# Kernel optimization log

Measured on AMD Instinct MI355X. Metric: run time of the kernel, lower is better.

The kernel has to match this reference:

```python
import jax, jax.numpy as jnp
import numpy as np


def _dsepconv(inp, vertical, horizontal, offset_x, offset_y, mask):
    # inp: [B,C,H,W]; vertical/horizontal: [B,F,H,W]; offset_x/offset_y/mask: [B,F*F,H,W]
    B, C, H, W = inp.shape
    F_ = min(vertical.shape[1], horizontal.shape[1])
    T = F_ * F_
    out_h = min(vertical.shape[2], horizontal.shape[2])
    out_w = min(vertical.shape[3], horizontal.shape[3])

    fy = jnp.repeat(jnp.arange(F_), F_).astype(inp.dtype)   # [T] tap row index
    fx = jnp.tile(jnp.arange(F_), F_).astype(inp.dtype)     # [T] tap col index
    h_idx = jnp.arange(out_h, dtype=inp.dtype)
    w_idx = jnp.arange(out_w, dtype=inp.dtype)
    c_off = (F_ - 1) / 2.0

    # NOTE: original code uses offset_y for the x coordinate and offset_x for y (faithful swap)
    x_norm = 2.0 * (offset_y + w_idx[None, None, None, :] + fx[None, :, None, None] - c_off + 1.0) / W - 1.0
    y_norm = 2.0 * (offset_x + h_idx[None, None, :, None] + fy[None, :, None, None] - c_off + 1.0) / H - 1.0
    x_norm = jnp.clip(x_norm, -1.0, 1.0)
    y_norm = jnp.clip(y_norm, -1.0, 1.0)

    # grid_sample align_corners=False mapping to pixel coords
    ix = ((x_norm + 1.0) * W - 1.0) / 2.0   # [B,T,H,W]
    iy = ((y_norm + 1.0) * H - 1.0) / 2.0

    x0 = jnp.floor(ix)
    y0 = jnp.floor(iy)
    wx1 = ix - x0  # fractional weights
    wy1 = iy - y0
    wx0 = 1.0 - wx1
    wy0 = 1.0 - wy1

    # border padding: clamp integer neighbor indices
    x0i = jnp.clip(x0.astype(jnp.int32), 0, W - 1)
    x1i = jnp.clip(x0.astype(jnp.int32) + 1, 0, W - 1)
    y0i = jnp.clip(y0.astype(jnp.int32), 0, H - 1)
    y1i = jnp.clip(y0.astype(jnp.int32) + 1, 0, H - 1)

    def gather(img, yi, xi):  # img [C,H,W], yi/xi [T,h,w] -> [C,T,h,w]
        return img[:, yi, xi]
    g = jax.vmap(gather)  # over batch -> [B,C,T,h,w]

    # combined per-tap coefficient: vertical[fy] * horizontal[fx] * mask[tap]
    coef = (vertical[:, jnp.repeat(jnp.arange(F_), F_), :out_h, :out_w]
            * horizontal[:, jnp.tile(jnp.arange(F_), F_), :out_h, :out_w]
            * mask[:, :, :out_h, :out_w])  # [B,T,h,w]

    out = (jnp.einsum('bthw,bcthw->bchw', coef * wy0 * wx0, g(inp, y0i, x0i))
           + jnp.einsum('bthw,bcthw->bchw', coef * wy0 * wx1, g(inp, y0i, x1i))
           + jnp.einsum('bthw,bcthw->bchw', coef * wy1 * wx0, g(inp, y1i, x0i))
           + jnp.einsum('bthw,bcthw->bchw', coef * wy1 * wx1, g(inp, y1i, x1i)))
    return out


def setup_inputs() -> dict:
    key = jax.random.key(0)
    k = jax.random.split(key, 6)
    B, C, H, W, F_ = 2, 3, 512, 512, 5
    T = F_ * F_
    return {
        'tensorInput': jax.random.normal(k[0], (B, C, H, W), dtype=jnp.float32),
        'tensorVertical': jax.random.uniform(k[1], (B, F_, H, W), dtype=jnp.float32),
        'tensorHorizontal': jax.random.uniform(k[2], (B, F_, H, W), dtype=jnp.float32),
        'tensorOffsetX': jax.random.normal(k[3], (B, T, H, W), dtype=jnp.float32),
        'tensorOffsetY': jax.random.normal(k[4], (B, T, H, W), dtype=jnp.float32),
        'tensorMask': jax.random.uniform(k[5], (B, T, H, W), dtype=jnp.float32),
    }


def reference(tensorInput, tensorVertical, tensorHorizontal, tensorOffsetX, tensorOffsetY, tensorMask):
    return _dsepconv(tensorInput, tensorVertical, tensorHorizontal, tensorOffsetX, tensorOffsetY, tensorMask)
```

## Files before the change

### kernel.cpp

```cpp
#include <hip/hip_runtime.h>

#define B_ 2
#define C_ 3
#define H_ 512
#define W_ 512
#define F_ 5
#define T_ 25
#define HW_ (H_ * W_)
#define PW_ 520
#define PH_ 513

#define NT(p) __builtin_nontemporal_load(p)

typedef _Float16 h4 __attribute__((ext_vector_type(4), aligned(8)));
typedef _Float16 h8 __attribute__((ext_vector_type(8), aligned(8)));

__global__ __launch_bounds__(256) void repack_kernel(
    const float* __restrict__ inp, h4* __restrict__ pk)
{
    const int x   = (blockIdx.x << 8) + threadIdx.x;
    const int row = blockIdx.y;
    const int b   = blockIdx.z;
    const int sr  = row < H_ ? row : H_ - 1;
    const float* p = inp + b * (C_ * HW_) + (sr << 9) + x;
    h4 v;
    v.x = (_Float16)p[0];
    v.y = (_Float16)p[HW_];
    v.z = (_Float16)p[2 * HW_];
    v.w = (_Float16)0.f;
    h4* dst = pk + b * (PH_ * PW_) + row * PW_;
    dst[x] = v;
    if (x == W_ - 1) dst[W_] = v;
}

__global__ __launch_bounds__(256) void dsepconv_kernel(
    const h4* __restrict__ pk,
    const float* __restrict__ vert,
    const float* __restrict__ horz,
    const float* __restrict__ offx,
    const float* __restrict__ offy,
    const float* __restrict__ mask,
    float* __restrict__ out)
{
    const int idx = blockIdx.x * blockDim.x + threadIdx.x;
    const int w = idx & (W_ - 1);
    const int h = (idx >> 9) & (H_ - 1);
    const int b = idx >> 18;

    const int hw = (h << 9) | w;

    const float* vb   = vert + b * (F_ * HW_) + hw;
    const float* hb   = horz + b * (F_ * HW_) + hw;
    const float* ob_x = offx + b * (T_ * HW_) + hw;
    const float* ob_y = offy + b * (T_ * HW_) + hw;
    const float* mb   = mask + b * (T_ * HW_) + hw;
    const h4* pb      = pk + b * (PH_ * PW_);

    float v[F_], hz[F_];
#pragma unroll
    for (int f = 0; f < F_; ++f) v[f]  = NT(vb + f * HW_);
#pragma unroll
    for (int f = 0; f < F_; ++f) hz[f] = NT(hb + f * HW_);

    float acc0 = 0.f, acc1 = 0.f, acc2 = 0.f;

    const float wf = (float)w;
    const float hf = (float)h;

    float cy[F_], cx[F_], cm[F_];
#pragma unroll
    for (int fx = 0; fx < F_; ++fx) {
        cy[fx] = NT(ob_y + fx * HW_);
        cx[fx] = NT(ob_x + fx * HW_);
        cm[fx] = NT(mb   + fx * HW_);
    }

#pragma unroll
    for (int fy = 0; fy < F_; ++fy) {
        float ny[F_], nx[F_], nm[F_];
        if (fy < F_ - 1) {
#pragma unroll
            for (int fx = 0; fx < F_; ++fx) {
                const int t = (fy + 1) * F_ + fx;
                ny[fx] = NT(ob_y + t * HW_);
                nx[fx] = NT(ob_x + t * HW_);
                nm[fx] = NT(mb   + t * HW_);
            }
        }

        const float vfy = v[fy];
        const float fyf = (float)fy;

#pragma unroll
        for (int fx = 0; fx < F_; ++fx) {
            const float oy = cy[fx];
            const float ox = cx[fx];
            const float m  = cm[fx];

            float ixf = oy + (wf + (float)fx - 1.5f);
            float iyf = ox + (hf + fyf       - 1.5f);
            ixf = fminf(fmaxf(ixf, -0.5f), (float)W_ - 0.5f);
            iyf = fminf(fmaxf(iyf, -0.5f), (float)H_ - 0.5f);

            float x0f = floorf(ixf), y0f = floorf(iyf);
            float wx1 = (x0f < 0.f) ? 0.f : (ixf - x0f);
            float wy1 = (y0f < 0.f) ? 0.f : (iyf - y0f);
            float wx0 = 1.0f - wx1;

            const int xb = (int)fmaxf(x0f, 0.f);
            const int yb = (int)fmaxf(y0f, 0.f);

            const h8 gt = *(const h8*)(pb + yb * PW_ + xb);
            const h8 gb = *(const h8*)(pb + (yb + 1) * PW_ + xb);

            const float coef = vfy * hz[fx] * m;
            const float cw0 = coef * (1.0f - wy1);
            const float cw1 = coef * wy1;

            const float t0 = wx0 * (float)gt[0] + wx1 * (float)gt[4];
            const float t1 = wx0 * (float)gt[1] + wx1 * (float)gt[5];
            const float t2 = wx0 * (float)gt[2] + wx1 * (float)gt[6];
            const float b0 = wx0 * (float)gb[0] + wx1 * (float)gb[4];
            const float b1 = wx0 * (float)gb[1] + wx1 * (float)gb[5];
            const float b2 = wx0 * (float)gb[2] + wx1 * (float)gb[6];

            acc0 += cw0 * t0 + cw1 * b0;
            acc1 += cw0 * t1 + cw1 * b1;
            acc2 += cw0 * t2 + cw1 * b2;
        }

        if (fy < F_ - 1) {
#pragma unroll
            for (int fx = 0; fx < F_; ++fx) {
                cy[fx] = ny[fx];
                cx[fx] = nx[fx];
                cm[fx] = nm[fx];
            }
        }
    }

    float* ob = out + b * (C_ * HW_) + hw;
    __builtin_nontemporal_store(acc0, ob);
    __builtin_nontemporal_store(acc1, ob + HW_);
    __builtin_nontemporal_store(acc2, ob + 2 * HW_);
}

extern "C" void kernel_launch(void* const* d_in, const int* in_sizes, int n_in,
                              void* d_out, int out_size, void* d_ws, size_t ws_size,
                              hipStream_t stream) {
    const float* inp  = (const float*)d_in[0];
    const float* vert = (const float*)d_in[1];
    const float* horz = (const float*)d_in[2];
    const float* offx = (const float*)d_in[3];
    const float* offy = (const float*)d_in[4];
    const float* mask = (const float*)d_in[5];
    float* out = (float*)d_out;
    h4* pk = (h4*)d_ws;

    dim3 blockR(256), gridR(W_ / 256, PH_, B_);
    hipLaunchKernelGGL(repack_kernel, gridR, blockR, 0, stream, inp, pk);

    const int total = B_ * H_ * W_;
    dim3 block(256), grid(total / 256);
    hipLaunchKernelGGL(dsepconv_kernel, grid, block, 0, stream,
                       pk, vert, horz, offx, offy, mask, out);
}
```

Before: 207.3 us.

## Stage input halo tile in LDS for bilinear gathers with global fallback

The kernel now runs on a 2D grid of 64x4 pixel blocks. Each block first copies a 25x88 packed fp16 halo region of the input into shared memory, then serves the bilinear corner gathers from LDS, falling back to global memory when a sampled offset lands outside the halo. The goal is to replace scattered global/L2 gathers with LDS reads. In exchange it adds a tile-load phase, a barrier, about 17.6KB of LDS per block and divergent fallback branches. It also raises the launch bounds minimum occupancy hint.

```diff
diff --git a/kernel.cpp b/kernel.cpp
--- a/kernel.cpp
+++ b/kernel.cpp
@@ -10,10 +10,17 @@
 #define PW_ 520
 #define PH_ 513
 
+#define TBW 64
+#define TBH 4
+#define RY  10
+#define RX  10
+#define TRH (TBH + 2 * RY + 1)
+#define TCW 88
+#define TILE_N (TRH * TCW)
+
 #define NT(p) __builtin_nontemporal_load(p)
 
 typedef _Float16 h4 __attribute__((ext_vector_type(4), aligned(8)));
-typedef _Float16 h8 __attribute__((ext_vector_type(8), aligned(8)));
 
 __global__ __launch_bounds__(256) void repack_kernel(
     const float* __restrict__ inp, h4* __restrict__ pk)
@@ -33,7 +40,7 @@
     if (x == W_ - 1) dst[W_] = v;
 }
 
-__global__ __launch_bounds__(256) void dsepconv_kernel(
+__global__ __launch_bounds__(256, 4) void dsepconv_kernel(
     const h4* __restrict__ pk,
     const float* __restrict__ vert,
     const float* __restrict__ horz,
@@ -42,10 +49,15 @@
     const float* __restrict__ mask,
     float* __restrict__ out)
 {
-    const int idx = blockIdx.x * blockDim.x + threadIdx.x;
-    const int w = idx & (W_ - 1);
-    const int h = (idx >> 9) & (H_ - 1);
-    const int b = idx >> 18;
+    __shared__ h4 tile[TILE_N];
+
+    const int tid  = threadIdx.x;
+    const int lane = tid & 63;
+    const int h0   = blockIdx.y * TBH;
+    const int w0b  = blockIdx.x * TBW;
+    const int b    = blockIdx.z;
+    const int h    = h0 + (tid >> 6);
+    const int w    = w0b + lane;
 
     const int hw = (h << 9) | w;
 
@@ -62,11 +74,6 @@
 #pragma unroll
     for (int f = 0; f < F_; ++f) hz[f] = NT(hb + f * HW_);
 
-    float acc0 = 0.f, acc1 = 0.f, acc2 = 0.f;
-
-    const float wf = (float)w;
-    const float hf = (float)h;
-
     float cy[F_], cx[F_], cm[F_];
 #pragma unroll
     for (int fx = 0; fx < F_; ++fx) {
@@ -74,6 +81,22 @@
         cx[fx] = NT(ob_x + fx * HW_);
         cm[fx] = NT(mb   + fx * HW_);
     }
+
+    for (int j = tid; j < TILE_N; j += 256) {
+        const int r  = j / TCW;
+        const int c  = j - r * TCW;
+        const int gr = min(max(h0 - RY + r, 0), H_);
+        const int gc = min(max(w0b - RX + c, 0), W_);
+        tile[j] = pb[gr * PW_ + gc];
+    }
+    __syncthreads();
+
+    float acc0 = 0.f, acc1 = 0.f, acc2 = 0.f;
+
+    const float wf = (float)w;
+    const float hf = (float)h;
+    const int hm = h0 - RY;
+    const int wm = w0b - RX;
 
 #pragma unroll
     for (int fy = 0; fy < F_; ++fy) {
@@ -110,23 +133,34 @@
             const int xb = (int)fmaxf(x0f, 0.f);
             const int yb = (int)fmaxf(y0f, 0.f);
 
-            const h8 gt = *(const h8*)(pb + yb * PW_ + xb);
-            const h8 gb = *(const h8*)(pb + (yb + 1) * PW_ + xb);
+            const int ty = yb - hm;
+            const int tc = xb - wm;
+
+            h4 t00, t01, t10, t11;
+            if (__builtin_expect((unsigned)ty < (TRH - 1) && (unsigned)tc < (TCW - 1), 1)) {
+                const h4* p = &tile[ty * TCW + tc];
+                t00 = p[0];
+                t01 = p[1];
+                t10 = p[TCW];
+                t11 = p[TCW + 1];
+            } else {
+                const h4* gp = pb + yb * PW_ + xb;
+                t00 = gp[0];
+                t01 = gp[1];
+                t10 = gp[PW_];
+                t11 = gp[PW_ + 1];
+            }
 
             const float coef = vfy * hz[fx] * m;
             const float cw0 = coef * (1.0f - wy1);
             const float cw1 = coef * wy1;
 
-            const float t0 = wx0 * (float)gt[0] + wx1 * (float)gt[4];
-            const float t1 = wx0 * (float)gt[1] + wx1 * (float)gt[5];
-            const float t2 = wx0 * (float)gt[2] + wx1 * (float)gt[6];
-            const float b0 = wx0 * (float)gb[0] + wx1 * (float)gb[4];
-            const float b1 = wx0 * (float)gb[1] + wx1 * (float)gb[5];
-            const float b2 = wx0 * (float)gb[2] + wx1 * (float)gb[6];
-
-            acc0 += cw0 * t0 + cw1 * b0;
-            acc1 += cw0 * t1 + cw1 * b1;
-            acc2 += cw0 * t2 + cw1 * b2;
+            acc0 += cw0 * (wx0 * (float)t00.x + wx1 * (float)t01.x)
+                  + cw1 * (wx0 * (float)t10.x + wx1 * (float)t11.x);
+            acc1 += cw0 * (wx0 * (float)t00.y + wx1 * (float)t01.y)
+                  + cw1 * (wx0 * (float)t10.y + wx1 * (float)t11.y);
+            acc2 += cw0 * (wx0 * (float)t00.z + wx1 * (float)t01.z)
+                  + cw1 * (wx0 * (float)t10.z + wx1 * (float)t11.z);
         }
 
         if (fy < F_ - 1) {
@@ -160,8 +194,8 @@
     dim3 blockR(256), gridR(W_ / 256, PH_, B_);
     hipLaunchKernelGGL(repack_kernel, gridR, blockR, 0, stream, inp, pk);
 
-    const int total = B_ * H_ * W_;
-    dim3 block(256), grid(total / 256);
+    dim3 block(256);
+    dim3 grid(W_ / TBW, H_ / TBH, B_);
     hipLaunchKernelGGL(dsepconv_kernel, grid, block, 0, stream,
                        pk, vert, horz, offx, offy, mask, out);
 }
```

After: 440.6 us. 2.13x slower.

## Do bilinear interpolation in packed fp16 and drop manual load prefetching

Applied to the files above, without the earlier changes.

The bilinear blend of the four gathered pixels now runs as packed half-precision vector math: horizontal lerp, then vertical lerp, then one fp32 multiply by the tap coefficient per channel. The manual double-buffering of next-row offset and mask loads is removed, so each row's loads are issued just before use. Launch bounds now request 4 waves per SIMD to limit register use. This aims to cut ALU work and register pressure, in exchange for fp16 rounding in the interpolation weights and sums, and possibly less latency hiding on the streaming loads.

```diff
diff --git a/kernel.cpp b/kernel.cpp
--- a/kernel.cpp
+++ b/kernel.cpp
@@ -33,7 +33,7 @@
     if (x == W_ - 1) dst[W_] = v;
 }
 
-__global__ __launch_bounds__(256) void dsepconv_kernel(
+__global__ __launch_bounds__(256, 4) void dsepconv_kernel(
     const h4* __restrict__ pk,
     const float* __restrict__ vert,
     const float* __restrict__ horz,
@@ -54,7 +54,7 @@
     const float* ob_x = offx + b * (T_ * HW_) + hw;
     const float* ob_y = offy + b * (T_ * HW_) + hw;
     const float* mb   = mask + b * (T_ * HW_) + hw;
-    const h4* pb      = pk + b * (PH_ * PW_);
+    const h8* pb      = (const h8*)(pk + b * (PH_ * PW_));
 
     float v[F_], hz[F_];
 #pragma unroll
@@ -67,25 +67,15 @@
     const float wf = (float)w;
     const float hf = (float)h;
 
-    float cy[F_], cx[F_], cm[F_];
-#pragma unroll
-    for (int fx = 0; fx < F_; ++fx) {
-        cy[fx] = NT(ob_y + fx * HW_);
-        cx[fx] = NT(ob_x + fx * HW_);
-        cm[fx] = NT(mb   + fx * HW_);
-    }
-
 #pragma unroll
     for (int fy = 0; fy < F_; ++fy) {
-        float ny[F_], nx[F_], nm[F_];
-        if (fy < F_ - 1) {
+        float cy[F_], cx[F_], cm[F_];
 #pragma unroll
-            for (int fx = 0; fx < F_; ++fx) {
-                const int t = (fy + 1) * F_ + fx;
-                ny[fx] = NT(ob_y + t * HW_);
-                nx[fx] = NT(ob_x + t * HW_);
-                nm[fx] = NT(mb   + t * HW_);
-            }
+        for (int fx = 0; fx < F_; ++fx) {
+            const int t = fy * F_ + fx;
+            cy[fx] = NT(ob_y + t * HW_);
+            cx[fx] = NT(ob_x + t * HW_);
+            cm[fx] = NT(mb   + t * HW_);
         }
 
         const float vfy = v[fy];
@@ -105,37 +95,35 @@
             float x0f = floorf(ixf), y0f = floorf(iyf);
             float wx1 = (x0f < 0.f) ? 0.f : (ixf - x0f);
             float wy1 = (y0f < 0.f) ? 0.f : (iyf - y0f);
-            float wx0 = 1.0f - wx1;
 
             const int xb = (int)fmaxf(x0f, 0.f);
             const int yb = (int)fmaxf(y0f, 0.f);
 
-            const h8 gt = *(const h8*)(pb + yb * PW_ + xb);
-            const h8 gb = *(const h8*)(pb + (yb + 1) * PW_ + xb);
+            const h8 gt = *(const h8*)((const h4*)pb + yb * PW_ + xb);
+            const h8 gb = *(const h8*)((const h4*)pb + (yb + 1) * PW_ + xb);
+
+            const _Float16 wx1h = (_Float16)wx1;
+            const _Float16 wx0h = (_Float16)1.f - wx1h;
+            const _Float16 wy1h = (_Float16)wy1;
+            const _Float16 wy0h = (_Float16)1.f - wy1h;
+            const h4 wx0v = { wx0h, wx0h, wx0h, wx0h };
+            const h4 wx1v = { wx1h, wx1h, wx1h, wx1h };
+            const h4 wy0v = { wy0h, wy0h, wy0h, wy0h };
+            const h4 wy1v = { wy1h, wy1h, wy1h, wy1h };
+
+            const h4 t0 = __builtin_shufflevector(gt, gt, 0, 1, 2, 3);
+            const h4 t1 = __builtin_shufflevector(gt, gt, 4, 5, 6, 7);
+            const h4 b0 = __builtin_shufflevector(gb, gb, 0, 1, 2, 3);
+            const h4 b1 = __builtin_shufflevector(gb, gb, 4, 5, 6, 7);
+
+            const h4 rt = t0 * wx0v + t1 * wx1v;
+            const h4 rb = b0 * wx0v + b1 * wx1v;
+            const h4 r  = rt * wy0v + rb * wy1v;
 
             const float coef = vfy * hz[fx] * m;
-            const float cw0 = coef * (1.0f - wy1);
-            const float cw1 = coef * wy1;
-
-            const float t0 = wx0 * (float)gt[0] + wx1 * (float)gt[4];
-            const float t1 = wx0 * (float)gt[1] + wx1 * (float)gt[5];
-            const float t2 = wx0 * (float)gt[2] + wx1 * (float)gt[6];
-            const float b0 = wx0 * (float)gb[0] + wx1 * (float)gb[4];
-            const float b1 = wx0 * (float)gb[1] + wx1 * (float)gb[5];
-            const float b2 = wx0 * (float)gb[2] + wx1 * (float)gb[6];
-
-            acc0 += cw0 * t0 + cw1 * b0;
-            acc1 += cw0 * t1 + cw1 * b1;
-            acc2 += cw0 * t2 + cw1 * b2;
-        }
-
-        if (fy < F_ - 1) {
-#pragma unroll
-            for (int fx = 0; fx < F_; ++fx) {
-                cy[fx] = ny[fx];
-                cx[fx] = nx[fx];
-                cm[fx] = nm[fx];
-            }
+            acc0 += coef * (float)r.x;
+            acc1 += coef * (float)r.y;
+            acc2 += coef * (float)r.z;
         }
     }
 
```

Measured after the change: 210.5 us. Within noise of the previous version (+1.5%).
